# Kernel tuning notes

Hardware: AMD Instinct MI355X
Metric: run time of the kernel (lower is better)

The kernel has to match this reference:

```python
import jax, jax.numpy as jnp
import numpy as np

B, LIN, E, D, N = 32, 2048, 512, 512, 2  # batch, enc len, enc hidden, dec hidden, dec layers


def setup_inputs() -> dict:
    key = jax.random.key(0)
    k1, k2, k3, k4, k5 = jax.random.split(key, 5)
    d_hidden = jax.random.normal(k1, (B, N, D), dtype=jnp.float32)
    encoder_outputs = jax.random.normal(k2, (B, LIN, E), dtype=jnp.float32)
    fan_in = E + N * D
    lim1 = 1.0 / np.sqrt(fan_in)
    W1 = jax.random.uniform(k3, (fan_in, D), minval=-lim1, maxval=lim1, dtype=jnp.float32)
    b1 = jax.random.uniform(k4, (D,), minval=-lim1, maxval=lim1, dtype=jnp.float32)
    lim2 = 1.0 / np.sqrt(D)
    w2 = jax.random.uniform(k5, (D,), minval=-lim2, maxval=lim2, dtype=jnp.float32)
    return {"d_hidden": d_hidden, "encoder_outputs": encoder_outputs,
            "W1": W1, "b1": b1, "w2": w2}


def reference(d_hidden, encoder_outputs, W1, b1, w2):
    # Faithful to: tanh(Linear(cat(repeat(d_hidden), enc))) -> Linear(.,1) -> softmax
    # cat@W1 == d_flat@W1_d + enc@W1_e (broadcast-add avoids materializing the concat).
    nd = d_hidden.shape[1] * d_hidden.shape[2]
    d_flat = d_hidden.reshape(d_hidden.shape[0], nd)        # [B, N*D]
    W1_d, W1_e = W1[:nd], W1[nd:]                            # [N*D,D], [E,D]
    dec_proj = d_flat @ W1_d + b1                            # [B, D]
    enc_proj = jnp.einsum('ble,ed->bld', encoder_outputs, W1_e)  # [B, Lin, D]
    attn_hidden = jnp.tanh(enc_proj + dec_proj[:, None, :])  # [B, Lin, D]
    scores = jnp.einsum('bld,d->bl', attn_hidden, w2)        # [B, Lin]
    return jax.nn.softmax(scores, axis=-1)
```

## Files before the change

### kernel.cpp

```cpp
#include <hip/hip_runtime.h>
#include <hip/hip_bf16.h>

#define L_SZ 2048
#define E_SZ 512
#define D_SZ 512
#define ND   1024
#define WS_DEC_OFF 0
#define WS_BT_OFF  (32*512*4)
#define WS_SC_OFF  (32*512*4 + 512*512*2)

typedef unsigned short ushort_t;
typedef unsigned int   uint_t;
typedef __attribute__((ext_vector_type(8))) short short8;
typedef __attribute__((ext_vector_type(4))) float floatx4;

__device__ __forceinline__ ushort_t f2bf(float f) {
  uint_t u = __builtin_bit_cast(uint_t, f);
  u += 0x7fffu + ((u >> 16) & 1u);
  return (ushort_t)(u >> 16);
}

__device__ __forceinline__ float fast_tanh(float x) {
  float e = __expf(2.0f * x);
  return 1.0f - 2.0f * __builtin_amdgcn_rcpf(e + 1.0f);
}

__device__ __forceinline__ void dma16(const ushort_t* g, ushort_t* l) {
  __builtin_amdgcn_global_load_lds(
      (const __attribute__((address_space(1))) uint_t*)(const void*)g,
      (__attribute__((address_space(3))) uint_t*)(void*)l,
      16, 0, 0);
}

__global__ __launch_bounds__(256) void prep_k(const float* __restrict__ dh,
                                              const float* __restrict__ W1,
                                              const float* __restrict__ b1,
                                              float* __restrict__ dec,
                                              ushort_t* __restrict__ Bt) {
  int blk = blockIdx.x, t = threadIdx.x;
  if (blk < 256) {
    int b = blk >> 3, d = (blk & 7) * 64 + (t & 63);
    int q = t >> 6;
    __shared__ float red[4][64];
    const float* dfb = dh + b * ND;
    float s = 0.f;
    #pragma unroll 8
    for (int k = q * 256; k < q * 256 + 256; k++)
      s = fmaf(dfb[k], W1[k * D_SZ + d], s);
    red[q][t & 63] = s;
    __syncthreads();
    if (q == 0)
      dec[b * D_SZ + d] = red[0][t] + red[1][t] + red[2][t] + red[3][t] + b1[d];
  } else {
    int tid = blk - 256;
    int tk = (tid >> 4) * 32, tn = (tid & 15) * 32;
    __shared__ float tile[32][33];
    int cc = t & 31, r8 = t >> 5;
    #pragma unroll
    for (int p = 0; p < 4; p++) {
      int r = r8 + p * 8;
      tile[r][cc] = W1[(ND + tk + r) * D_SZ + tn + cc];
    }
    __syncthreads();
    #pragma unroll
    for (int p = 0; p < 4; p++) {
      int nn = r8 + p * 8;
      Bt[(tn + nn) * E_SZ + tk + cc] = f2bf(tile[cc][nn]);
    }
  }
}

__global__ __launch_bounds__(512, 4) void main_k(const float* __restrict__ enc,
                                                 const ushort_t* __restrict__ Bt,
                                                 const float* __restrict__ dec,
                                                 const float* __restrict__ w2,
                                                 float* __restrict__ scores) {
  const int b  = blockIdx.y;
  const int l0 = blockIdx.x * 64;
  const int t  = threadIdx.x;
  const int wave = t >> 6, lane = t & 63;
  const int col = lane & 15, quad = lane >> 4;

  __shared__ ushort_t As[64 * 64];
  __shared__ ushort_t Bs[512 * 64];
  __shared__ float s_sc[64];

  if (t < 64) s_sc[t] = 0.f;

  floatx4 acc[4][4];
  #pragma unroll
  for (int mt = 0; mt < 4; mt++)
    #pragma unroll
    for (int nt = 0; nt < 4; nt++)
      acc[mt][nt] = (floatx4){0.f, 0.f, 0.f, 0.f};

  const float* arow = enc + (size_t)(b * L_SZ + l0) * E_SZ;

  const int am = t >> 3, ac = t & 7;
  const float* aptr = arow + am * E_SZ + ac * 8;
  ushort_t* awr = &As[am * 64 + ((ac ^ (am & 7)) << 3)];

  const int bn0 = wave * 64 + (lane >> 3);
  const int bc0 = (lane & 7) ^ ((lane >> 3) & 7);
  const ushort_t* bptr0 = Bt + bn0 * E_SZ + bc0 * 8;

  float4 pa = *(const float4*)aptr;
  float4 pb = *(const float4*)(aptr + 4);

  #pragma unroll 1
  for (int kw = 0; kw < 8; kw++) {
    __syncthreads();
    union { short8 v; __hip_bfloat162 h[4]; } pk;
    pk.h[0] = __float22bfloat162_rn(make_float2(pa.x, pa.y));
    pk.h[1] = __float22bfloat162_rn(make_float2(pa.z, pa.w));
    pk.h[2] = __float22bfloat162_rn(make_float2(pb.x, pb.y));
    pk.h[3] = __float22bfloat162_rn(make_float2(pb.z, pb.w));
    *(short8*)awr = pk.v;
    const ushort_t* bp = bptr0 + kw * 64;
    #pragma unroll
    for (int j = 0; j < 8; j++)
      dma16(bp + j * 8 * E_SZ, &Bs[(wave * 512 + j * 64) * 8]);
    __syncthreads();
    if (kw < 7) {
      const float* ap = aptr + (kw + 1) * 64;
      pa = *(const float4*)ap;
      pb = *(const float4*)(ap + 4);
    }
    #pragma unroll
    for (int ks = 0; ks < 2; ks++) {
      short8 af[4], bfr[4];
      #pragma unroll
      for (int mt = 0; mt < 4; mt++) {
        int m = mt * 16 + col;
        af[mt] = *(const short8*)&As[m * 64 + ((((ks << 2) + quad) ^ (m & 7)) << 3)];
      }
      #pragma unroll
      for (int nt = 0; nt < 4; nt++) {
        int n = wave * 64 + nt * 16 + col;
        bfr[nt] = *(const short8*)&Bs[n * 64 + ((((ks << 2) + quad) ^ (n & 7)) << 3)];
      }
      #pragma unroll
      for (int mt = 0; mt < 4; mt++)
        #pragma unroll
        for (int nt = 0; nt < 4; nt++)
          acc[mt][nt] = __builtin_amdgcn_mfma_f32_16x16x32_bf16(af[mt], bfr[nt], acc[mt][nt], 0, 0, 0);
    }
  }

  const float* decb = dec + b * D_SZ;
  float sums[4][4];
  #pragma unroll
  for (int mt = 0; mt < 4; mt++)
    #pragma unroll
    for (int r = 0; r < 4; r++) sums[mt][r] = 0.f;

  #pragma unroll
  for (int nt = 0; nt < 4; nt++) {
    int n = wave * 64 + nt * 16 + col;
    float dv = decb[n];
    float wv = w2[n];
    #pragma unroll
    for (int mt = 0; mt < 4; mt++)
      #pragma unroll
      for (int r = 0; r < 4; r++)
        sums[mt][r] += fast_tanh(acc[mt][nt][r] + dv) * wv;
  }
  #pragma unroll
  for (int mt = 0; mt < 4; mt++) {
    #pragma unroll
    for (int r = 0; r < 4; r++) {
      float v = sums[mt][r];
      v += __shfl_xor(v, 1, 16);
      v += __shfl_xor(v, 2, 16);
      v += __shfl_xor(v, 4, 16);
      v += __shfl_xor(v, 8, 16);
      if (col == 0) atomicAdd(&s_sc[mt * 16 + quad * 4 + r], v);
    }
  }
  __syncthreads();
  if (t < 64) scores[b * L_SZ + l0 + t] = s_sc[t];
}

__global__ __launch_bounds__(1024) void softmax_k(const float* __restrict__ sc,
                                                  float* __restrict__ out) {
  int b = blockIdx.x, t = threadIdx.x;
  int wave = t >> 6, lane = t & 63;
  __shared__ float redm[16], reds[16];
  const float* row = sc + b * L_SZ;
  float v0 = row[t], v1 = row[t + 1024];
  float mx = fmaxf(v0, v1);
  #pragma unroll
  for (int off = 32; off >= 1; off >>= 1) mx = fmaxf(mx, __shfl_xor(mx, off, 64));
  if (lane == 0) redm[wave] = mx;
  __syncthreads();
  float m = redm[0];
  #pragma unroll
  for (int i = 1; i < 16; i++) m = fmaxf(m, redm[i]);
  v0 = __expf(v0 - m);
  v1 = __expf(v1 - m);
  float s = v0 + v1;
  #pragma unroll
  for (int off = 32; off >= 1; off >>= 1) s += __shfl_xor(s, off, 64);
  if (lane == 0) reds[wave] = s;
  __syncthreads();
  float sum = reds[0];
  #pragma unroll
  for (int i = 1; i < 16; i++) sum += reds[i];
  float inv = 1.0f / sum;
  out[b * L_SZ + t]        = v0 * inv;
  out[b * L_SZ + t + 1024] = v1 * inv;
}

extern "C" void kernel_launch(void* const* d_in, const int* in_sizes, int n_in,
                              void* d_out, int out_size, void* d_ws, size_t ws_size,
                              hipStream_t stream) {
  const float* d_hidden = (const float*)d_in[0];
  const float* enc      = (const float*)d_in[1];
  const float* W1       = (const float*)d_in[2];
  const float* b1       = (const float*)d_in[3];
  const float* w2       = (const float*)d_in[4];
  float* out = (float*)d_out;

  char* ws = (char*)d_ws;
  float*    dec = (float*)(ws + WS_DEC_OFF);
  ushort_t* Bt  = (ushort_t*)(ws + WS_BT_OFF);
  float*    sc  = (float*)(ws + WS_SC_OFF);

  prep_k<<<512, 256, 0, stream>>>(d_hidden, W1, b1, dec, Bt);
  main_k<<<dim3(32, 32), 512, 0, stream>>>(enc, Bt, dec, w2, sc);
  softmax_k<<<32, 1024, 0, stream>>>(sc, out);
}
```

Measured before the change: 235.7 us.

## Load B fragments directly from global into registers and double-buffer A tile

```diff
diff --git a/kernel.cpp b/kernel.cpp
--- a/kernel.cpp
+++ b/kernel.cpp
@@ -23,13 +23,6 @@
 __device__ __forceinline__ float fast_tanh(float x) {
   float e = __expf(2.0f * x);
   return 1.0f - 2.0f * __builtin_amdgcn_rcpf(e + 1.0f);
-}
-
-__device__ __forceinline__ void dma16(const ushort_t* g, ushort_t* l) {
-  __builtin_amdgcn_global_load_lds(
-      (const __attribute__((address_space(1))) uint_t*)(const void*)g,
-      (__attribute__((address_space(3))) uint_t*)(void*)l,
-      16, 0, 0);
 }
 
 __global__ __launch_bounds__(256) void prep_k(const float* __restrict__ dh,
@@ -81,8 +74,7 @@
   const int wave = t >> 6, lane = t & 63;
   const int col = lane & 15, quad = lane >> 4;
 
-  __shared__ ushort_t As[64 * 64];
-  __shared__ ushort_t Bs[512 * 64];
+  __shared__ __align__(16) ushort_t As[2][64 * 64];
   __shared__ float s_sc[64];
 
   if (t < 64) s_sc[t] = 0.f;
@@ -98,53 +90,71 @@
 
   const int am = t >> 3, ac = t & 7;
   const float* aptr = arow + am * E_SZ + ac * 8;
-  ushort_t* awr = &As[am * 64 + ((ac ^ (am & 7)) << 3)];
-
-  const int bn0 = wave * 64 + (lane >> 3);
-  const int bc0 = (lane & 7) ^ ((lane >> 3) & 7);
-  const ushort_t* bptr0 = Bt + bn0 * E_SZ + bc0 * 8;
+  const int awoff = am * 64 + ((ac ^ (am & 7)) << 3);
+
+  const ushort_t* bp0 = Bt + (wave * 64 + col) * E_SZ + quad * 8;
+  const ushort_t* bp1 = bp0 + 16 * E_SZ;
+  const ushort_t* bp2 = bp0 + 32 * E_SZ;
+  const ushort_t* bp3 = bp0 + 48 * E_SZ;
 
   float4 pa = *(const float4*)aptr;
   float4 pb = *(const float4*)(aptr + 4);
 
-  #pragma unroll 1
-  for (int kw = 0; kw < 8; kw++) {
-    __syncthreads();
+  {
     union { short8 v; __hip_bfloat162 h[4]; } pk;
     pk.h[0] = __float22bfloat162_rn(make_float2(pa.x, pa.y));
     pk.h[1] = __float22bfloat162_rn(make_float2(pa.z, pa.w));
     pk.h[2] = __float22bfloat162_rn(make_float2(pb.x, pb.y));
     pk.h[3] = __float22bfloat162_rn(make_float2(pb.z, pb.w));
-    *(short8*)awr = pk.v;
-    const ushort_t* bp = bptr0 + kw * 64;
-    #pragma unroll
-    for (int j = 0; j < 8; j++)
-      dma16(bp + j * 8 * E_SZ, &Bs[(wave * 512 + j * 64) * 8]);
-    __syncthreads();
+    *(short8*)&As[0][awoff] = pk.v;
+  }
+  {
+    const float* ap = aptr + 64;
+    pa = *(const float4*)ap;
+    pb = *(const float4*)(ap + 4);
+  }
+  __syncthreads();
+
+  #pragma unroll 1
+  for (int kw = 0; kw < 8; kw++) {
+    short8 bfr[8];
+    bfr[0] = *(const short8*)(bp0);  bfr[4] = *(const short8*)(bp0 + 32);
+    bfr[1] = *(const short8*)(bp1);  bfr[5] = *(const short8*)(bp1 + 32);
+    bfr[2] = *(const short8*)(bp2);  bfr[6] = *(const short8*)(bp2 + 32);
+    bfr[3] = *(const short8*)(bp3);  bfr[7] = *(const short8*)(bp3 + 32);
+    bp0 += 64; bp1 += 64; bp2 += 64; bp3 += 64;
+
     if (kw < 7) {
-      const float* ap = aptr + (kw + 1) * 64;
-      pa = *(const float4*)ap;
-      pb = *(const float4*)(ap + 4);
-    }
+      union { short8 v; __hip_bfloat162 h[4]; } pk;
+      pk.h[0] = __float22bfloat162_rn(make_float2(pa.x, pa.y));
+      pk.h[1] = __float22bfloat162_rn(make_float2(pa.z, pa.w));
+      pk.h[2] = __float22bfloat162_rn(make_float2(pb.x, pb.y));
+      pk.h[3] = __float22bfloat162_rn(make_float2(pb.z, pb.w));
+      *(short8*)&As[(kw + 1) & 1][awoff] = pk.v;
+      if (kw < 6) {
+        const float* ap = aptr + (kw + 2) * 64;
+        pa = *(const float4*)ap;
+        pb = *(const float4*)(ap + 4);
+      }
+    }
+
+    const ushort_t* Acur = &As[kw & 1][0];
     #pragma unroll
     for (int ks = 0; ks < 2; ks++) {
-      short8 af[4], bfr[4];
+      short8 af[4];
       #pragma unroll
       for (int mt = 0; mt < 4; mt++) {
         int m = mt * 16 + col;
-        af[mt] = *(const short8*)&As[m * 64 + ((((ks << 2) + quad) ^ (m & 7)) << 3)];
-      }
-      #pragma unroll
-      for (int nt = 0; nt < 4; nt++) {
-        int n = wave * 64 + nt * 16 + col;
-        bfr[nt] = *(const short8*)&Bs[n * 64 + ((((ks << 2) + quad) ^ (n & 7)) << 3)];
+        af[mt] = *(const short8*)&Acur[m * 64 + ((((ks << 2) + quad) ^ (m & 7)) << 3)];
       }
       #pragma unroll
       for (int mt = 0; mt < 4; mt++)
         #pragma unroll
         for (int nt = 0; nt < 4; nt++)
-          acc[mt][nt] = __builtin_amdgcn_mfma_f32_16x16x32_bf16(af[mt], bfr[nt], acc[mt][nt], 0, 0, 0);
-    }
+          acc[mt][nt] = __builtin_amdgcn_mfma_f32_16x16x32_bf16(af[mt], bfr[ks * 4 + nt], acc[mt][nt], 0, 0, 0);
+    }
+
+    __syncthreads();
   }
 
   const float* decb = dec + b * D_SZ;
```

Result: slower. 258.9 us (+9.8%).

## Double-buffer A and B LDS tiles to overlap next-step loads with MFMA

Applied to the files above, without the earlier changes.

```diff
diff --git a/kernel.cpp b/kernel.cpp
--- a/kernel.cpp
+++ b/kernel.cpp
@@ -70,7 +70,7 @@
   }
 }
 
-__global__ __launch_bounds__(512, 4) void main_k(const float* __restrict__ enc,
+__global__ __launch_bounds__(512, 2) void main_k(const float* __restrict__ enc,
                                                  const ushort_t* __restrict__ Bt,
                                                  const float* __restrict__ dec,
                                                  const float* __restrict__ w2,
@@ -81,8 +81,8 @@
   const int wave = t >> 6, lane = t & 63;
   const int col = lane & 15, quad = lane >> 4;
 
-  __shared__ ushort_t As[64 * 64];
-  __shared__ ushort_t Bs[512 * 64];
+  __shared__ __align__(16) ushort_t Bs[2][512 * 64];
+  __shared__ __align__(16) ushort_t As[2][64 * 64];
   __shared__ float s_sc[64];
 
   if (t < 64) s_sc[t] = 0.f;
@@ -98,7 +98,7 @@
 
   const int am = t >> 3, ac = t & 7;
   const float* aptr = arow + am * E_SZ + ac * 8;
-  ushort_t* awr = &As[am * 64 + ((ac ^ (am & 7)) << 3)];
+  const int awoff = am * 64 + ((ac ^ (am & 7)) << 3);
 
   const int bn0 = wave * 64 + (lane >> 3);
   const int bc0 = (lane & 7) ^ ((lane >> 3) & 7);
@@ -106,38 +106,49 @@
 
   float4 pa = *(const float4*)aptr;
   float4 pb = *(const float4*)(aptr + 4);
-
-  #pragma unroll 1
-  for (int kw = 0; kw < 8; kw++) {
-    __syncthreads();
+  #pragma unroll
+  for (int j = 0; j < 8; j++)
+    dma16(bptr0 + j * 8 * E_SZ, &Bs[0][wave * 4096 + j * 512]);
+  {
     union { short8 v; __hip_bfloat162 h[4]; } pk;
     pk.h[0] = __float22bfloat162_rn(make_float2(pa.x, pa.y));
     pk.h[1] = __float22bfloat162_rn(make_float2(pa.z, pa.w));
     pk.h[2] = __float22bfloat162_rn(make_float2(pb.x, pb.y));
     pk.h[3] = __float22bfloat162_rn(make_float2(pb.z, pb.w));
-    *(short8*)awr = pk.v;
-    const ushort_t* bp = bptr0 + kw * 64;
-    #pragma unroll
-    for (int j = 0; j < 8; j++)
-      dma16(bp + j * 8 * E_SZ, &Bs[(wave * 512 + j * 64) * 8]);
-    __syncthreads();
+    *(short8*)&As[0][awoff] = pk.v;
+  }
+  asm volatile("s_waitcnt vmcnt(0) lgkmcnt(0)" ::: "memory");
+  __builtin_amdgcn_s_barrier();
+  __builtin_amdgcn_sched_barrier(0);
+
+  #pragma unroll 1
+  for (int kw = 0; kw < 8; kw++) {
+    const ushort_t* Acur = &As[kw & 1][0];
+    const ushort_t* Bcur = &Bs[kw & 1][0];
+
     if (kw < 7) {
       const float* ap = aptr + (kw + 1) * 64;
       pa = *(const float4*)ap;
       pb = *(const float4*)(ap + 4);
-    }
+      const ushort_t* bp = bptr0 + (kw + 1) * 64;
+      ushort_t* bld = &Bs[(kw + 1) & 1][wave * 4096];
+      #pragma unroll
+      for (int j = 0; j < 8; j++)
+        dma16(bp + j * 8 * E_SZ, bld + j * 512);
+    }
+
     #pragma unroll
     for (int ks = 0; ks < 2; ks++) {
       short8 af[4], bfr[4];
       #pragma unroll
       for (int mt = 0; mt < 4; mt++) {
         int m = mt * 16 + col;
-        af[mt] = *(const short8*)&As[m * 64 + ((((ks << 2) + quad) ^ (m & 7)) << 3)];
+        af[mt] = *(const short8*)&Acur[m * 64 + ((((ks << 2) + quad) ^ (m & 7)) << 3)];
       }
       #pragma unroll
       for (int nt = 0; nt < 4; nt++) {
         int n = wave * 64 + nt * 16 + col;
-        bfr[nt] = *(const short8*)&Bs[n * 64 + ((((ks << 2) + quad) ^ (n & 7)) << 3)];
+        bfr[nt] = *(const short8*)&Bcur[n * 64 + ((((ks << 2) + quad) ^ (n & 7)) << 3)];
       }
       #pragma unroll
       for (int mt = 0; mt < 4; mt++)
@@ -145,6 +156,19 @@
         for (int nt = 0; nt < 4; nt++)
           acc[mt][nt] = __builtin_amdgcn_mfma_f32_16x16x32_bf16(af[mt], bfr[nt], acc[mt][nt], 0, 0, 0);
     }
+
+    if (kw < 7) {
+      union { short8 v; __hip_bfloat162 h[4]; } pk;
+      pk.h[0] = __float22bfloat162_rn(make_float2(pa.x, pa.y));
+      pk.h[1] = __float22bfloat162_rn(make_float2(pa.z, pa.w));
+      pk.h[2] = __float22bfloat162_rn(make_float2(pb.x, pb.y));
+      pk.h[3] = __float22bfloat162_rn(make_float2(pb.z, pb.w));
+      *(short8*)&As[(kw + 1) & 1][awoff] = pk.v;
+    }
+
+    asm volatile("s_waitcnt vmcnt(0) lgkmcnt(0)" ::: "memory");
+    __builtin_amdgcn_s_barrier();
+    __builtin_amdgcn_sched_barrier(0);
   }
 
   const float* decb = dec + b * D_SZ;
```

After: 263.9 us. 1.12x slower.

## Stage full A tile in LDS once and stream B fragments from global

Applied to the files above, without the earlier changes.

```diff
diff --git a/kernel.cpp b/kernel.cpp
--- a/kernel.cpp
+++ b/kernel.cpp
@@ -23,13 +23,6 @@
 __device__ __forceinline__ float fast_tanh(float x) {
   float e = __expf(2.0f * x);
   return 1.0f - 2.0f * __builtin_amdgcn_rcpf(e + 1.0f);
-}
-
-__device__ __forceinline__ void dma16(const ushort_t* g, ushort_t* l) {
-  __builtin_amdgcn_global_load_lds(
-      (const __attribute__((address_space(1))) uint_t*)(const void*)g,
-      (__attribute__((address_space(3))) uint_t*)(void*)l,
-      16, 0, 0);
 }
 
 __global__ __launch_bounds__(256) void prep_k(const float* __restrict__ dh,
@@ -81,8 +74,7 @@
   const int wave = t >> 6, lane = t & 63;
   const int col = lane & 15, quad = lane >> 4;
 
-  __shared__ ushort_t As[64 * 64];
-  __shared__ ushort_t Bs[512 * 64];
+  __shared__ __align__(16) ushort_t As[64 * 512];
   __shared__ float s_sc[64];
 
   if (t < 64) s_sc[t] = 0.f;
@@ -96,54 +88,64 @@
 
   const float* arow = enc + (size_t)(b * L_SZ + l0) * E_SZ;
 
-  const int am = t >> 3, ac = t & 7;
-  const float* aptr = arow + am * E_SZ + ac * 8;
-  ushort_t* awr = &As[am * 64 + ((ac ^ (am & 7)) << 3)];
-
-  const int bn0 = wave * 64 + (lane >> 3);
-  const int bc0 = (lane & 7) ^ ((lane >> 3) & 7);
-  const ushort_t* bptr0 = Bt + bn0 * E_SZ + bc0 * 8;
-
-  float4 pa = *(const float4*)aptr;
-  float4 pb = *(const float4*)(aptr + 4);
+  #pragma unroll
+  for (int j = 0; j < 8; j++) {
+    int c = t + j * 512;
+    int kw = c >> 8, mt = (c >> 6) & 3, q = (c >> 4) & 3, cl = c & 15;
+    const float* gp = arow + (mt * 16 + cl) * E_SZ + kw * 32 + q * 8;
+    float4 f0 = *(const float4*)gp;
+    float4 f1 = *(const float4*)(gp + 4);
+    union { short8 v; __hip_bfloat162 h[4]; } pk;
+    pk.h[0] = __float22bfloat162_rn(make_float2(f0.x, f0.y));
+    pk.h[1] = __float22bfloat162_rn(make_float2(f0.z, f0.w));
+    pk.h[2] = __float22bfloat162_rn(make_float2(f1.x, f1.y));
+    pk.h[3] = __float22bfloat162_rn(make_float2(f1.z, f1.w));
+    *(short8*)&As[c * 8] = pk.v;
+  }
+  __syncthreads();
+
+  const ushort_t* bb0 = Bt + (wave * 64 +  0 + col) * E_SZ + quad * 8;
+  const ushort_t* bb1 = Bt + (wave * 64 + 16 + col) * E_SZ + quad * 8;
+  const ushort_t* bb2 = Bt + (wave * 64 + 32 + col) * E_SZ + quad * 8;
+  const ushort_t* bb3 = Bt + (wave * 64 + 48 + col) * E_SZ + quad * 8;
+
+  short8 b0[4], b1[4];
+  b0[0] = *(const short8*)bb0;
+  b0[1] = *(const short8*)bb1;
+  b0[2] = *(const short8*)bb2;
+  b0[3] = *(const short8*)bb3;
 
   #pragma unroll 1
-  for (int kw = 0; kw < 8; kw++) {
-    __syncthreads();
-    union { short8 v; __hip_bfloat162 h[4]; } pk;
-    pk.h[0] = __float22bfloat162_rn(make_float2(pa.x, pa.y));
-    pk.h[1] = __float22bfloat162_rn(make_float2(pa.z, pa.w));
-    pk.h[2] = __float22bfloat162_rn(make_float2(pb.x, pb.y));
-    pk.h[3] = __float22bfloat162_rn(make_float2(pb.z, pb.w));
-    *(short8*)awr = pk.v;
-    const ushort_t* bp = bptr0 + kw * 64;
-    #pragma unroll
-    for (int j = 0; j < 8; j++)
-      dma16(bp + j * 8 * E_SZ, &Bs[(wave * 512 + j * 64) * 8]);
-    __syncthreads();
-    if (kw < 7) {
-      const float* ap = aptr + (kw + 1) * 64;
-      pa = *(const float4*)ap;
-      pb = *(const float4*)(ap + 4);
-    }
-    #pragma unroll
-    for (int ks = 0; ks < 2; ks++) {
-      short8 af[4], bfr[4];
+  for (int kw2 = 0; kw2 < 16; kw2 += 2) {
+    {
+      const int off = (kw2 + 1) * 32;
+      b1[0] = *(const short8*)(bb0 + off);
+      b1[1] = *(const short8*)(bb1 + off);
+      b1[2] = *(const short8*)(bb2 + off);
+      b1[3] = *(const short8*)(bb3 + off);
       #pragma unroll
       for (int mt = 0; mt < 4; mt++) {
-        int m = mt * 16 + col;
-        af[mt] = *(const short8*)&As[m * 64 + ((((ks << 2) + quad) ^ (m & 7)) << 3)];
+        short8 af = *(const short8*)&As[(kw2 * 256 + mt * 64 + quad * 16 + col) * 8];
+        #pragma unroll
+        for (int nt = 0; nt < 4; nt++)
+          acc[mt][nt] = __builtin_amdgcn_mfma_f32_16x16x32_bf16(af, b0[nt], acc[mt][nt], 0, 0, 0);
+      }
+    }
+    {
+      if (kw2 < 14) {
+        const int off = (kw2 + 2) * 32;
+        b0[0] = *(const short8*)(bb0 + off);
+        b0[1] = *(const short8*)(bb1 + off);
+        b0[2] = *(const short8*)(bb2 + off);
+        b0[3] = *(const short8*)(bb3 + off);
       }
       #pragma unroll
-      for (int nt = 0; nt < 4; nt++) {
-        int n = wave * 64 + nt * 16 + col;
-        bfr[nt] = *(const short8*)&Bs[n * 64 + ((((ks << 2) + quad) ^ (n & 7)) << 3)];
-      }
-      #pragma unroll
-      for (int mt = 0; mt < 4; mt++)
+      for (int mt = 0; mt < 4; mt++) {
+        short8 af = *(const short8*)&As[((kw2 + 1) * 256 + mt * 64 + quad * 16 + col) * 8];
         #pragma unroll
         for (int nt = 0; nt < 4; nt++)
-          acc[mt][nt] = __builtin_amdgcn_mfma_f32_16x16x32_bf16(af[mt], bfr[nt], acc[mt][nt], 0, 0, 0);
+          acc[mt][nt] = __builtin_amdgcn_mfma_f32_16x16x32_bf16(af, b1[nt], acc[mt][nt], 0, 0, 0);
+      }
     }
   }
 
```

After: 273.7 us. 1.16x slower.
